# Kernel optimization log

Measured on AMD Instinct MI355X. Metric: run time of the kernel, lower is better.

Reference implementation:

```python
import jax, jax.numpy as jnp
import numpy as np
import math
from jax import lax

B, T, D, K, H, MLP_DIM, WIN = 4, 2048, 1024, 64, 4, 4096, 128
KH = K // H          # eigenstates per head
HD = D // H          # attention head dim


def layer_norm(x, g, b, eps=1e-5):
    mu = jnp.mean(x, axis=-1, keepdims=True)
    var = jnp.mean(jnp.square(x - mu), axis=-1, keepdims=True)
    return (x - mu) * lax.rsqrt(var + eps) * g + b


def setup_inputs() -> dict:
    key = jax.random.key(0)
    ks = jax.random.split(key, 16)
    s = 0.02
    # layer_idx=1, n_layers=6 -> depth_ratio=0.2, decay_center=-1.7
    return {
        "x": jax.random.normal(ks[0], (B, T, D), jnp.float32),
        "prev_eigenstates": jax.random.normal(ks[1], (B, T, 2 * K), jnp.float32),
        "norm1_g": jnp.ones((D,), jnp.float32),
        "norm1_b": jnp.zeros((D,), jnp.float32),
        "in_proj_w": jax.random.normal(ks[2], (2 * K, D), jnp.float32) * s,
        "memory_gate": jnp.array(-3.0, jnp.float32),
        "memory_proj_w": jnp.eye(2 * K, dtype=jnp.float32),
        "log_decay": jax.random.uniform(ks[3], (K,), jnp.float32, -2.7, -1.2),
        "frequency": jnp.linspace(0.0, 2 * math.pi * (1 - 1 / K), K, dtype=jnp.float32),
        "coupling": jnp.tile(jnp.eye(KH, dtype=jnp.float32), (H, 1, 1))
                    + 0.01 * jax.random.normal(ks[4], (H, KH, KH), jnp.float32) / math.sqrt(KH),
        "main_gate_w": jax.random.normal(ks[5], (D, D), jnp.float32) * s,
        "main_gate_b": jnp.full((D,), -2.0, jnp.float32),
        "out_proj_w": jax.random.normal(ks[6], (D, 2 * K), jnp.float32) * s,
        "attn_norm_g": jnp.ones((D,), jnp.float32),
        "attn_norm_b": jnp.zeros((D,), jnp.float32),
        "attn_in_w": jax.random.normal(ks[7], (3 * D, D), jnp.float32) * s,
        "attn_in_b": jnp.zeros((3 * D,), jnp.float32),
        "attn_out_w": jax.random.normal(ks[8], (D, D), jnp.float32) * s,
        "attn_out_b": jnp.zeros((D,), jnp.float32),
        "norm2_g": jnp.ones((D,), jnp.float32),
        "norm2_b": jnp.zeros((D,), jnp.float32),
        "mlp_w1": jax.random.normal(ks[9], (MLP_DIM, D), jnp.float32) * s,
        "mlp_b1": jnp.zeros((MLP_DIM,), jnp.float32),
        "mlp_w2": jax.random.normal(ks[10], (D, MLP_DIM), jnp.float32) * s,
        "mlp_b2": jnp.zeros((D,), jnp.float32),
    }


def eigenstate_fft(log_decay, frequency, beta_r, beta_i):
    # diagonal complex SSM recurrence: c_t = lam * c_{t-1} + beta_t
    lam = jnp.exp(log_decay)
    lr = lam * jnp.cos(frequency)   # (K,)
    li = lam * jnp.sin(frequency)
    br = jnp.transpose(beta_r, (1, 0, 2))  # (T,B,K)
    bi = jnp.transpose(beta_i, (1, 0, 2))

    def step(carry, inp):
        sr, si = carry
        xr, xi = inp
        nr = lr * sr - li * si + xr
        ni = lr * si + li * sr + xi
        return (nr, ni), (nr, ni)

    init = (jnp.zeros(br.shape[1:], br.dtype), jnp.zeros(bi.shape[1:], bi.dtype))
    _, (cr, ci) = lax.scan(step, init, (br, bi))
    return jnp.transpose(cr, (1, 0, 2)), jnp.transpose(ci, (1, 0, 2))


def reference(x, prev_eigenstates, norm1_g, norm1_b, in_proj_w, memory_gate,
              memory_proj_w, log_decay, frequency, coupling, main_gate_w,
              main_gate_b, out_proj_w, attn_norm_g, attn_norm_b, attn_in_w,
              attn_in_b, attn_out_w, attn_out_b, norm2_g, norm2_b,
              mlp_w1, mlp_b1, mlp_w2, mlp_b2):
    b, t, d = x.shape
    residual = x
    x_norm = layer_norm(x, norm1_g, norm1_b)

    beta = jnp.einsum('btd,kd->btk', x_norm, in_proj_w)        # (B,T,2K)
    beta_r, beta_i = jnp.split(beta, 2, axis=-1)

    # cross-layer memory
    mg = jax.nn.sigmoid(memory_gate)
    prev = jnp.einsum('btk,jk->btj', prev_eigenstates, memory_proj_w)
    pr, pi = jnp.split(prev, 2, axis=-1)
    beta_r = beta_r + mg * pr
    beta_i = beta_i + mg * pi

    c_r, c_i = eigenstate_fft(log_decay, frequency, beta_r, beta_i)  # (B,T,K)

    # per-head coupling
    c_r_h = c_r.reshape(b, t, H, KH)
    c_i_h = c_i.reshape(b, t, H, KH)
    c_r = jnp.einsum('hjk,bthk->bthj', coupling, c_r_h).reshape(b, t, K)
    c_i = jnp.einsum('hjk,bthk->bthj', coupling, c_i_h).reshape(b, t, K)
    eigenstates_out = jnp.concatenate([c_r, c_i], axis=-1)     # (B,T,2K)

    h = jnp.einsum('btk,dk->btd', eigenstates_out, out_proj_w)
    # spectral gate (band gates computed in torch are unused in the output)
    main_g = jax.nn.sigmoid(jnp.einsum('btd,ed->bte', x_norm, main_gate_w) + main_gate_b)
    h = main_g * h
    x = residual + h

    # sliding-window attention (dense masked MHA, as in the source)
    attn_in = layer_norm(x, attn_norm_g, attn_norm_b)
    qkv = jnp.einsum('btd,ed->bte', attn_in, attn_in_w) + attn_in_b
    q, k_, v = jnp.split(qkv, 3, axis=-1)
    q = q.reshape(b, t, H, HD).transpose(0, 2, 1, 3)           # (B,H,T,hd)
    k_ = k_.reshape(b, t, H, HD).transpose(0, 2, 1, 3)
    v = v.reshape(b, t, H, HD).transpose(0, 2, 1, 3)
    scale = 1.0 / math.sqrt(HD)
    scores = jnp.einsum('bhqd,bhkd->bhqk', q, k_) * scale
    idx = jnp.arange(t)
    diff = idx[:, None] - idx[None, :]
    allowed = (diff >= 0) & (diff <= WIN)                      # True = attend
    scores = jnp.where(allowed, scores, jnp.finfo(scores.dtype).min)
    attn = jax.nn.softmax(scores, axis=-1)
    ao = jnp.einsum('bhqk,bhkd->bhqd', attn, v)
    ao = ao.transpose(0, 2, 1, 3).reshape(b, t, d)
    ao = jnp.einsum('btd,ed->bte', ao, attn_out_w) + attn_out_b
    x = x + ao

    # MLP
    x2 = layer_norm(x, norm2_g, norm2_b)
    m = jax.nn.silu(jnp.einsum('btd,md->btm', x2, mlp_w1) + mlp_b1)
    m = jnp.einsum('btm,dm->btd', m, mlp_w2) + mlp_b2
    x = x + m
    return (x, eigenstates_out)
```

## Files before the change

### kernel.cpp

```cpp
#include <hip/hip_runtime.h>


typedef __bf16 bf16_t;
typedef bf16_t bf16x8 __attribute__((ext_vector_type(8)));
typedef bf16_t bf16x4 __attribute__((ext_vector_type(4)));
typedef float  f32x4  __attribute__((ext_vector_type(4)));

#define Tc   2048
#define Dc   1024
#define BTc  8192
#define K2c  128
#define MLPc 4096

struct ConvSeg { const float* src; bf16_t* dst; int n; };
struct ConvArgs { ConvSeg s[9]; };

__global__ __launch_bounds__(256) void convert_kernel(ConvArgs a) {
    ConvSeg sg = a.s[blockIdx.y];
    int i = (blockIdx.x * 256 + threadIdx.x) * 4;
    if (i >= sg.n) return;
    float4 v = *(const float4*)(sg.src + i);
    bf16x4 o;
    o[0] = (bf16_t)v.x; o[1] = (bf16_t)v.y; o[2] = (bf16_t)v.z; o[3] = (bf16_t)v.w;
    *(bf16x4*)(sg.dst + i) = o;
}

__global__ __launch_bounds__(256) void ln_kernel(const float* __restrict__ x,
                                                 const float* __restrict__ g,
                                                 const float* __restrict__ bb,
                                                 bf16_t* __restrict__ out) {
    int row = blockIdx.x;
    int tid = threadIdx.x;
    float4 v = ((const float4*)(x + (size_t)row * Dc))[tid];
    float s  = v.x + v.y + v.z + v.w;
    float ss = v.x * v.x + v.y * v.y + v.z * v.z + v.w * v.w;
#pragma unroll
    for (int d = 32; d > 0; d >>= 1) {
        s  += __shfl_down(s, d);
        ss += __shfl_down(ss, d);
    }
    __shared__ float red[8];
    int wv = tid >> 6;
    if ((tid & 63) == 0) { red[wv] = s; red[4 + wv] = ss; }
    __syncthreads();
    s  = red[0] + red[1] + red[2] + red[3];
    ss = red[4] + red[5] + red[6] + red[7];
    float mean = s * (1.0f / Dc);
    float var  = ss * (1.0f / Dc) - mean * mean;
    float rstd = rsqrtf(var + 1e-5f);
    float4 g4 = ((const float4*)g)[tid];
    float4 b4 = ((const float4*)bb)[tid];
    bf16x4 o;
    o[0] = (bf16_t)((v.x - mean) * rstd * g4.x + b4.x);
    o[1] = (bf16_t)((v.y - mean) * rstd * g4.y + b4.y);
    o[2] = (bf16_t)((v.z - mean) * rstd * g4.z + b4.z);
    o[3] = (bf16_t)((v.w - mean) * rstd * g4.w + b4.w);
    *(bf16x4*)(out + (size_t)row * Dc + tid * 4) = o;
}

#define BM 128
#define BN 128
#define BK 32

struct EpiParams {
    const float* bias;
    float*       fout;
    const float* fin;
    bf16_t*      bout;
    bf16_t*      q; bf16_t* k; bf16_t* v;
    const bf16_t* a2; const bf16_t* w2;
};

#define GLOAD_LDS(g, l)                                                        \
    __builtin_amdgcn_global_load_lds(                                          \
        (const __attribute__((address_space(1))) unsigned int*)(g),            \
        (__attribute__((address_space(3))) unsigned int*)(l), 16, 0, 0)

template <int EPI>
__global__ __launch_bounds__(256) void gemm_tiled(const bf16_t* __restrict__ A,
                                                  const bf16_t* __restrict__ W,
                                                  int M, int N, int K,
                                                  EpiParams ep) {
    __shared__ bf16_t As[BM * BK];
    __shared__ bf16_t Bs[BN * BK];

    int tid = threadIdx.x;
    int wv = tid >> 6, lane = tid & 63;
    int lane16 = lane & 15, quad = lane >> 4;
    int nbn = N / BN;
    int bm = blockIdx.x / nbn, bn = blockIdx.x % nbn;
    int m0 = bm * BM, n0 = bn * BN;
    int wm = (wv >> 1) * 64, wn = (wv & 1) * 64;

    int lrow = lane >> 2;
    int lcol = (((lane & 3) ^ ((lrow >> 1) & 3))) * 8;
    const bf16_t* ga = A + (size_t)(m0 + wv * 16 + lrow) * K + lcol;
    const bf16_t* gb = W + (size_t)(n0 + wv * 16 + lrow) * K + lcol;
    size_t gstep64 = (size_t)64 * K;
    bf16_t* la0 = &As[(wv * 16) * BK];
    bf16_t* la1 = &As[(64 + wv * 16) * BK];
    bf16_t* lb0 = &Bs[(wv * 16) * BK];
    bf16_t* lb1 = &Bs[(64 + wv * 16) * BK];

    int pc = (quad ^ ((lane16 >> 1) & 3)) * 8;

    f32x4 zz = {0.f, 0.f, 0.f, 0.f};
    f32x4 acc[4][4];
#pragma unroll
    for (int mi = 0; mi < 4; mi++)
#pragma unroll
        for (int ni = 0; ni < 4; ni++) acc[mi][ni] = zz;

    for (int k0 = 0; k0 < K; k0 += BK) {
        GLOAD_LDS(ga + k0, la0);
        GLOAD_LDS(ga + k0 + gstep64, la1);
        GLOAD_LDS(gb + k0, lb0);
        GLOAD_LDS(gb + k0 + gstep64, lb1);
        __syncthreads();
        bf16x8 af[4], bfr[4];
#pragma unroll
        for (int mi = 0; mi < 4; mi++)
            af[mi] = *(const bf16x8*)&As[(wm + mi * 16 + lane16) * BK + pc];
#pragma unroll
        for (int ni = 0; ni < 4; ni++)
            bfr[ni] = *(const bf16x8*)&Bs[(wn + ni * 16 + lane16) * BK + pc];
#pragma unroll
        for (int mi = 0; mi < 4; mi++)
#pragma unroll
            for (int ni = 0; ni < 4; ni++)
                acc[mi][ni] = __builtin_amdgcn_mfma_f32_16x16x32_bf16(
                    af[mi], bfr[ni], acc[mi][ni], 0, 0, 0);
        __syncthreads();
    }

    f32x4 acc2[4][4];
    if constexpr (EPI == 6) {
#pragma unroll
        for (int mi = 0; mi < 4; mi++)
#pragma unroll
            for (int ni = 0; ni < 4; ni++) acc2[mi][ni] = zz;
        const bf16_t* ga2 = ep.a2 + (size_t)(m0 + wv * 16 + lrow) * K2c + lcol;
        const bf16_t* gb2 = ep.w2 + (size_t)(n0 + wv * 16 + lrow) * K2c + lcol;
        size_t gstep64b = (size_t)64 * K2c;
        for (int k0 = 0; k0 < K2c; k0 += BK) {
            GLOAD_LDS(ga2 + k0, la0);
            GLOAD_LDS(ga2 + k0 + gstep64b, la1);
            GLOAD_LDS(gb2 + k0, lb0);
            GLOAD_LDS(gb2 + k0 + gstep64b, lb1);
            __syncthreads();
            bf16x8 af[4], bfr[4];
#pragma unroll
            for (int mi = 0; mi < 4; mi++)
                af[mi] = *(const bf16x8*)&As[(wm + mi * 16 + lane16) * BK + pc];
#pragma unroll
            for (int ni = 0; ni < 4; ni++)
                bfr[ni] = *(const bf16x8*)&Bs[(wn + ni * 16 + lane16) * BK + pc];
#pragma unroll
            for (int mi = 0; mi < 4; mi++)
#pragma unroll
                for (int ni = 0; ni < 4; ni++)
                    acc2[mi][ni] = __builtin_amdgcn_mfma_f32_16x16x32_bf16(
                        af[mi], bfr[ni], acc2[mi][ni], 0, 0, 0);
            __syncthreads();
        }
    }

#pragma unroll
    for (int mi = 0; mi < 4; mi++)
#pragma unroll
        for (int ni = 0; ni < 4; ni++)
#pragma unroll
            for (int r = 0; r < 4; r++) {
                int row = m0 + wm + mi * 16 + quad * 4 + r;
                int col = n0 + wn + ni * 16 + lane16;
                float v = acc[mi][ni][r];
                if constexpr (EPI == 1) {
                    v += ep.bias[col];
                    ep.bout[(size_t)row * N + col] = (bf16_t)(v / (1.0f + __expf(-v)));
                } else if constexpr (EPI == 2) {
                    size_t o = (size_t)row * N + col;
                    ep.fout[o] = ep.fin[o] + v + ep.bias[col];
                } else if constexpr (EPI == 3) {
                    v += ep.bias[col];
                    int part = col >> 10, d1 = col & 1023;
                    int hh = d1 >> 8, hd = d1 & 255;
                    int b = row >> 11, t = row & 2047;
                    bf16_t* dst = (part == 0) ? ep.q : ep.k;
                    dst[(((size_t)(b * 4 + hh) * Tc + t) << 8) + hd] = (bf16_t)v;
                } else if constexpr (EPI == 5) {
                    v += ep.bias[2048 + row];
                    int b = col >> 11, t = col & 2047;
                    int hh = row >> 8, dd = row & 255;
                    ep.v[((size_t)((b * 4 + hh) * 256 + dd)) * Tc + t] = (bf16_t)v;
                } else if constexpr (EPI == 6) {
                    size_t o = (size_t)row * N + col;
                    float g = 1.0f / (1.0f + __expf(-(v + ep.bias[col])));
                    ep.fout[o] = ep.fin[o] + g * acc2[mi][ni][r];
                }
            }
}

__device__ __forceinline__ void mm32(const bf16_t* __restrict__ A,
                                     const bf16_t* __restrict__ W,
                                     int K, int m0, int n0,
                                     int lane16, int quad, f32x4 (&acc)[2][2]) {
    const bf16_t* a0 = A + (size_t)(m0 + lane16) * K + quad * 8;
    const bf16_t* a1 = a0 + (size_t)16 * K;
    const bf16_t* w0 = W + (size_t)(n0 + lane16) * K + quad * 8;
    const bf16_t* w1 = w0 + (size_t)16 * K;
#pragma unroll 4
    for (int k = 0; k < K; k += 32) {
        bf16x8 av0 = *(const bf16x8*)(a0 + k);
        bf16x8 av1 = *(const bf16x8*)(a1 + k);
        bf16x8 bv0 = *(const bf16x8*)(w0 + k);
        bf16x8 bv1 = *(const bf16x8*)(w1 + k);
        acc[0][0] = __builtin_amdgcn_mfma_f32_16x16x32_bf16(av0, bv0, acc[0][0], 0, 0, 0);
        acc[0][1] = __builtin_amdgcn_mfma_f32_16x16x32_bf16(av0, bv1, acc[0][1], 0, 0, 0);
        acc[1][0] = __builtin_amdgcn_mfma_f32_16x16x32_bf16(av1, bv0, acc[1][0], 0, 0, 0);
        acc[1][1] = __builtin_amdgcn_mfma_f32_16x16x32_bf16(av1, bv1, acc[1][1], 0, 0, 0);
    }
}

__global__ __launch_bounds__(256) void gemm_beta(const bf16_t* __restrict__ xn,
                                                 const bf16_t* __restrict__ ipw,
                                                 const bf16_t* __restrict__ prevb,
                                                 const bf16_t* __restrict__ mpw,
                                                 const float* __restrict__ mgate_p,
                                                 float* __restrict__ beta_c) {
    int lane = threadIdx.x & 63;
    int wave = threadIdx.x >> 6;
    int gid  = blockIdx.x * 4 + wave;
    int mt = gid / 4, nt = gid % 4;
    int m0 = mt * 32, n0 = nt * 32;
    int lane16 = lane & 15, quad = lane >> 4;
    f32x4 zz = {0.f, 0.f, 0.f, 0.f};
    f32x4 acc[2][2] = {{zz, zz}, {zz, zz}};
    mm32(xn, ipw, Dc, m0, n0, lane16, quad, acc);
    f32x4 acc2[2][2] = {{zz, zz}, {zz, zz}};
    mm32(prevb, mpw, K2c, m0, n0, lane16, quad, acc2);
    float mg = 1.0f / (1.0f + __expf(-mgate_p[0]));
    for (int mi = 0; mi < 2; mi++)
        for (int ni = 0; ni < 2; ni++)
            for (int r = 0; r < 4; r++) {
                int row = m0 + mi * 16 + quad * 4 + r;
                int col = n0 + ni * 16 + lane16;
                int b = row >> 11, t = row & 2047;
                beta_c[((size_t)b * K2c + col) * Tc + t] =
                    acc[mi][ni][r] + mg * acc2[mi][ni][r];
            }
}

__global__ __launch_bounds__(64) void scan_kernel(const float* __restrict__ beta_c,
                                                  const float* __restrict__ log_decay,
                                                  const float* __restrict__ freq,
                                                  float* __restrict__ cbuf) {
    int b = blockIdx.x >> 6;
    int k = blockIdx.x & 63;
    int lane = threadIdx.x;
    float lam = expf(log_decay[k]);
    float fr = freq[k];
    float lr = lam * cosf(fr), li = lam * sinf(fr);

    const float* br_p = beta_c + ((size_t)b * K2c + k) * Tc + lane * 32;
    const float* bi_p = beta_c + ((size_t)b * K2c + 64 + k) * Tc + lane * 32;
    float br[32], bi[32];
#pragma unroll
    for (int i = 0; i < 8; i++) {
        *(float4*)(&br[i * 4]) = ((const float4*)br_p)[i];
        *(float4*)(&bi[i * 4]) = ((const float4*)bi_p)[i];
    }
    float sr = 0.f, si = 0.f;
#pragma unroll
    for (int i = 0; i < 32; i++) {
        float nr = lr * sr - li * si + br[i];
        float ni = lr * si + li * sr + bi[i];
        sr = nr; si = ni;
    }
    float Mr = lr, Mi = li;
#pragma unroll
    for (int i = 0; i < 5; i++) {
        float nr = Mr * Mr - Mi * Mi, ni = 2.f * Mr * Mi;
        Mr = nr; Mi = ni;
    }
    float ir = sr, ii = si;
#pragma unroll
    for (int d = 1; d < 64; d <<= 1) {
        float pr = __shfl_up(ir, d);
        float pi = __shfl_up(ii, d);
        if (lane >= d) {
            ir += Mr * pr - Mi * pi;
            ii += Mr * pi + Mi * pr;
        }
        float nr = Mr * Mr - Mi * Mi, ni = 2.f * Mr * Mi;
        Mr = nr; Mi = ni;
    }
    float cr = __shfl_up(ir, 1), ci = __shfl_up(ii, 1);
    if (lane == 0) { cr = 0.f; ci = 0.f; }
    float* cr_p = cbuf + ((size_t)b * K2c + k) * Tc + lane * 32;
    float* ci_p = cbuf + ((size_t)b * K2c + 64 + k) * Tc + lane * 32;
    sr = cr; si = ci;
#pragma unroll
    for (int i = 0; i < 32; i++) {
        float nr = lr * sr - li * si + br[i];
        float ni = lr * si + li * sr + bi[i];
        sr = nr; si = ni;
        cr_p[i] = sr; ci_p[i] = si;
    }
}

__global__ __launch_bounds__(256) void coupling_kernel(const float* __restrict__ cbuf,
                                                       const float* __restrict__ cpl,
                                                       float* __restrict__ eig_out,
                                                       bf16_t* __restrict__ eigb) {
    int idx = blockIdx.x * 256 + threadIdx.x;
    int col = idx & 127;
    int t = (idx >> 7) & 2047;
    int b = idx >> 18;
    int ri = col >> 6, hj = col & 63, h2 = hj >> 4, j = hj & 15;
    const float* crow = cbuf + ((size_t)b * K2c + ri * 64 + h2 * 16) * Tc + t;
    const float* cw = cpl + (h2 * 16 + j) * 16;
    float acc = 0.f;
#pragma unroll
    for (int kk = 0; kk < 16; kk++) acc += cw[kk] * crow[(size_t)kk * Tc];
    eig_out[idx] = acc;
    eigb[idx] = (bf16_t)acc;
}

#define LDP 168

__global__ __launch_bounds__(256) void attn_mfma(const bf16_t* __restrict__ qb,
                                                 const bf16_t* __restrict__ kb,
                                                 const bf16_t* __restrict__ vt,
                                                 bf16_t* __restrict__ ao) {
    __shared__ bf16_t Pl[4 * 16 * LDP];
    int tid = threadIdx.x;
    int wv = tid >> 6, lane = tid & 63;
    int lane16 = lane & 15, quad = lane >> 4;
    int qblk = blockIdx.x & 31;
    int bh = blockIdx.x >> 5;
    int qw0 = qblk * 64 + wv * 16;
    const bf16_t* qp = qb + (size_t)bh * Tc * 256;
    const bf16_t* kp = kb + (size_t)bh * Tc * 256;
    const bf16_t* vp = vt + (size_t)bh * 256 * Tc;
    bf16_t* Pw = &Pl[wv * 16 * LDP];

    for (int i = lane; i < 16 * 24; i += 64) {
        int r = i / 24, c = 144 + (i % 24);
        Pw[r * LDP + c] = (bf16_t)0.f;
    }

    bf16x8 qf[8];
#pragma unroll
    for (int ks = 0; ks < 8; ks++)
        qf[ks] = *(const bf16x8*)(qp + (size_t)(qw0 + lane16) * 256 + ks * 32 + quad * 8);

    f32x4 zz = {0.f, 0.f, 0.f, 0.f};
    f32x4 S[9];
#pragma unroll
    for (int jt = 0; jt < 9; jt++) S[jt] = zz;
    int kbase = qw0 - 128;

#pragma unroll
    for (int ks = 0; ks < 8; ks++) {
        bf16x8 kf[9];
#pragma unroll
        for (int jt = 0; jt < 9; jt++) {
            int krow = kbase + jt * 16 + lane16;
            krow = krow < 0 ? 0 : krow;
            kf[jt] = *(const bf16x8*)(kp + (size_t)krow * 256 + ks * 32 + quad * 8);
        }
#pragma unroll
        for (int jt = 0; jt < 9; jt++)
            S[jt] = __builtin_amdgcn_mfma_f32_16x16x32_bf16(qf[ks], kf[jt], S[jt], 0, 0, 0);
    }

    float m[4], l[4];
#pragma unroll
    for (int r = 0; r < 4; r++) m[r] = -1e30f;
#pragma unroll
    for (int jt = 0; jt < 9; jt++) {
        int kg = kbase + jt * 16 + lane16;
#pragma unroll
        for (int r = 0; r < 4; r++) {
            int qrow = qw0 + quad * 4 + r;
            bool ok = (kg >= 0) && (kg <= qrow) && (kg >= qrow - 128);
            float v = ok ? S[jt][r] * 0.0625f : -1e30f;
            S[jt][r] = v;
            m[r] = fmaxf(m[r], v);
        }
    }
#pragma unroll
    for (int d = 1; d < 16; d <<= 1)
#pragma unroll
        for (int r = 0; r < 4; r++)
            m[r] = fmaxf(m[r], __shfl_xor(m[r], d));
#pragma unroll
    for (int r = 0; r < 4; r++) l[r] = 0.f;
#pragma unroll
    for (int jt = 0; jt < 9; jt++)
#pragma unroll
        for (int r = 0; r < 4; r++) {
            float p = __expf(S[jt][r] - m[r]);
            S[jt][r] = p;
            l[r] += p;
        }
#pragma unroll
    for (int d = 1; d < 16; d <<= 1)
#pragma unroll
        for (int r = 0; r < 4; r++)
            l[r] += __shfl_xor(l[r], d);

#pragma unroll
    for (int jt = 0; jt < 9; jt++)
#pragma unroll
        for (int r = 0; r < 4; r++)
            Pw[(quad * 4 + r) * LDP + jt * 16 + lane16] = (bf16_t)S[jt][r];
    __syncthreads();

    f32x4 O[16];
#pragma unroll
    for (int nt = 0; nt < 16; nt++) O[nt] = zz;
#pragma unroll
    for (int ks = 0; ks < 5; ks++) {
        bf16x8 pf = *(const bf16x8*)&Pw[lane16 * LDP + ks * 32 + quad * 8];
        int kidx = kbase + ks * 32 + quad * 8;
        kidx = kidx < 0 ? 0 : kidx;
        kidx = kidx > (Tc - 8) ? (Tc - 8) : kidx;
#pragma unroll
        for (int nt = 0; nt < 16; nt++) {
            bf16x8 vf = *(const bf16x8*)(vp + (size_t)(nt * 16 + lane16) * Tc + kidx);
            O[nt] = __builtin_amdgcn_mfma_f32_16x16x32_bf16(pf, vf, O[nt], 0, 0, 0);
        }
    }

    float rl[4];
#pragma unroll
    for (int r = 0; r < 4; r++) rl[r] = 1.0f / l[r];
    int b = bh >> 2, h = bh & 3;
#pragma unroll
    for (int nt = 0; nt < 16; nt++)
#pragma unroll
        for (int r = 0; r < 4; r++) {
            int qrow = qw0 + quad * 4 + r;
            int dim = nt * 16 + lane16;
            ao[((size_t)(b * Tc + qrow)) * Dc + h * 256 + dim] = (bf16_t)(O[nt][r] * rl[r]);
        }
}

extern "C" void kernel_launch(void* const* d_in, const int* in_sizes, int n_in,
                              void* d_out, int out_size, void* d_ws, size_t ws_size,
                              hipStream_t stream) {
    const float* x            = (const float*)d_in[0];
    const float* prev_eig     = (const float*)d_in[1];
    const float* norm1_g      = (const float*)d_in[2];
    const float* norm1_b      = (const float*)d_in[3];
    const float* in_proj_w    = (const float*)d_in[4];
    const float* memory_gate  = (const float*)d_in[5];
    const float* memory_proj_w= (const float*)d_in[6];
    const float* log_decay    = (const float*)d_in[7];
    const float* frequency    = (const float*)d_in[8];
    const float* coupling     = (const float*)d_in[9];
    const float* main_gate_w  = (const float*)d_in[10];
    const float* main_gate_b  = (const float*)d_in[11];
    const float* out_proj_w   = (const float*)d_in[12];
    const float* attn_norm_g  = (const float*)d_in[13];
    const float* attn_norm_b  = (const float*)d_in[14];
    const float* attn_in_w    = (const float*)d_in[15];
    const float* attn_in_b    = (const float*)d_in[16];
    const float* attn_out_w   = (const float*)d_in[17];
    const float* attn_out_b   = (const float*)d_in[18];
    const float* norm2_g      = (const float*)d_in[19];
    const float* norm2_b      = (const float*)d_in[20];
    const float* mlp_w1       = (const float*)d_in[21];
    const float* mlp_b1       = (const float*)d_in[22];
    const float* mlp_w2       = (const float*)d_in[23];
    const float* mlp_b2       = (const float*)d_in[24];

    char* ws = (char*)d_ws;
    bf16_t* ipw_b  = (bf16_t*)(ws + 0);
    bf16_t* mpw_b  = (bf16_t*)(ws + 262144);
    bf16_t* mgw_b  = (bf16_t*)(ws + 294912);
    bf16_t* opw_b  = (bf16_t*)(ws + 2392064);
    bf16_t* aiw_b  = (bf16_t*)(ws + 2654208);
    bf16_t* aow_b  = (bf16_t*)(ws + 8945664);
    bf16_t* w1_b   = (bf16_t*)(ws + 11042816);
    bf16_t* w2_b   = (bf16_t*)(ws + 19431424);
    bf16_t* prev_b = (bf16_t*)(ws + 27820032);
    const size_t OFF_ACTA = 29917184;
    const size_t OFF_BIG  = OFF_ACTA + 16777216;
    bf16_t* actA   = (bf16_t*)(ws + OFF_ACTA);
    float*  beta_c = (float*)(ws + OFF_BIG);
    float*  cbuf   = (float*)(ws + OFF_BIG + 4194304);
    bf16_t* eigb   = (bf16_t*)(ws + OFF_BIG + 8388608);
    bf16_t* qbuf   = (bf16_t*)(ws + OFF_BIG);
    bf16_t* kbuf   = (bf16_t*)(ws + OFF_BIG + 16777216);
    bf16_t* vtbuf  = (bf16_t*)(ws + OFF_BIG + 33554432);
    bf16_t* mbuf   = (bf16_t*)(ws + OFF_BIG);

    float* out_x   = (float*)d_out;
    float* out_eig = out_x + (size_t)BTc * Dc;
    float* xres    = out_x;

    ConvArgs ca;
    ca.s[0] = ConvSeg{in_proj_w,     ipw_b,  131072};
    ca.s[1] = ConvSeg{memory_proj_w, mpw_b,  16384};
    ca.s[2] = ConvSeg{main_gate_w,   mgw_b,  1048576};
    ca.s[3] = ConvSeg{out_proj_w,    opw_b,  131072};
    ca.s[4] = ConvSeg{attn_in_w,     aiw_b,  3145728};
    ca.s[5] = ConvSeg{attn_out_w,    aow_b,  1048576};
    ca.s[6] = ConvSeg{mlp_w1,        w1_b,   4194304};
    ca.s[7] = ConvSeg{mlp_w2,        w2_b,   4194304};
    ca.s[8] = ConvSeg{prev_eig,      prev_b, 1048576};
    convert_kernel<<<dim3(4096, 9), 256, 0, stream>>>(ca);

    EpiParams ep{};

    ln_kernel<<<BTc, 256, 0, stream>>>(x, norm1_g, norm1_b, actA);
    gemm_beta<<<256, 256, 0, stream>>>(actA, ipw_b, prev_b, mpw_b, memory_gate, beta_c);
    scan_kernel<<<256, 64, 0, stream>>>(beta_c, log_decay, frequency, cbuf);
    coupling_kernel<<<4096, 256, 0, stream>>>(cbuf, coupling, out_eig, eigb);
    ep = EpiParams{}; ep.bias = main_gate_b; ep.fin = x; ep.fout = xres;
    ep.a2 = eigb; ep.w2 = opw_b;
    gemm_tiled<6><<<(BTc/BM)*(Dc/BN), 256, 0, stream>>>(actA, mgw_b, BTc, Dc, Dc, ep);
    ln_kernel<<<BTc, 256, 0, stream>>>(xres, attn_norm_g, attn_norm_b, actA);
    ep = EpiParams{}; ep.bias = attn_in_b; ep.q = qbuf; ep.k = kbuf;
    gemm_tiled<3><<<(BTc/BM)*(2048/BN), 256, 0, stream>>>(actA, aiw_b, BTc, 2048, Dc, ep);
    ep = EpiParams{}; ep.bias = attn_in_b; ep.v = vtbuf;
    gemm_tiled<5><<<(Dc/BM)*(BTc/BN), 256, 0, stream>>>(aiw_b + (size_t)2048 * Dc, actA,
                                                        Dc, BTc, Dc, ep);
    attn_mfma<<<512, 256, 0, stream>>>(qbuf, kbuf, vtbuf, actA);
    ep = EpiParams{}; ep.bias = attn_out_b; ep.fin = xres; ep.fout = xres;
    gemm_tiled<2><<<(BTc/BM)*(Dc/BN), 256, 0, stream>>>(actA, aow_b, BTc, Dc, Dc, ep);
    ln_kernel<<<BTc, 256, 0, stream>>>(xres, norm2_g, norm2_b, actA);
    ep = EpiParams{}; ep.bias = mlp_b1; ep.bout = mbuf;
    gemm_tiled<1><<<(BTc/BM)*(MLPc/BN), 256, 0, stream>>>(actA, w1_b, BTc, MLPc, Dc, ep);
    ep = EpiParams{}; ep.bias = mlp_b2; ep.fin = xres; ep.fout = out_x;
    gemm_tiled<2><<<(BTc/BM)*(Dc/BN), 256, 0, stream>>>(mbuf, w2_b, BTc, Dc, MLPc, ep);

    (void)in_sizes; (void)n_in; (void)out_size; (void)ws_size;
}
```

Measured before the change: 699.2 us.

## Double GEMM K-tile to 64 with 8-way XOR swizzle and XCD-aware block mapping

```diff
diff --git a/kernel.cpp b/kernel.cpp
--- a/kernel.cpp
+++ b/kernel.cpp
@@ -60,7 +60,7 @@
 
 #define BM 128
 #define BN 128
-#define BK 32
+#define BKT 64
 
 struct EpiParams {
     const float* bias;
@@ -81,28 +81,29 @@
                                                   const bf16_t* __restrict__ W,
                                                   int M, int N, int K,
                                                   EpiParams ep) {
-    __shared__ bf16_t As[BM * BK];
-    __shared__ bf16_t Bs[BN * BK];
+    __shared__ bf16_t As[BM * BKT];
+    __shared__ bf16_t Bs[BN * BKT];
 
     int tid = threadIdx.x;
     int wv = tid >> 6, lane = tid & 63;
     int lane16 = lane & 15, quad = lane >> 4;
-    int nbn = N / BN;
-    int bm = blockIdx.x / nbn, bn = blockIdx.x % nbn;
+    int nbn = N / BN, nbm = M / BM;
+
+    int bid = blockIdx.x;
+    int xcd = bid & 7;
+    int slot = bid >> 3;
+    int bm_per = nbm >> 3;
+    int bmo = slot / nbn;
+    int bno = slot % nbn;
+    if (bmo & 1) bno = nbn - 1 - bno;
+    int bm = xcd * bm_per + bmo, bn = bno;
     int m0 = bm * BM, n0 = bn * BN;
     int wm = (wv >> 1) * 64, wn = (wv & 1) * 64;
 
-    int lrow = lane >> 2;
-    int lcol = (((lane & 3) ^ ((lrow >> 1) & 3))) * 8;
-    const bf16_t* ga = A + (size_t)(m0 + wv * 16 + lrow) * K + lcol;
-    const bf16_t* gb = W + (size_t)(n0 + wv * 16 + lrow) * K + lcol;
-    size_t gstep64 = (size_t)64 * K;
-    bf16_t* la0 = &As[(wv * 16) * BK];
-    bf16_t* la1 = &As[(64 + wv * 16) * BK];
-    bf16_t* lb0 = &Bs[(wv * 16) * BK];
-    bf16_t* lb1 = &Bs[(64 + wv * 16) * BK];
-
-    int pc = (quad ^ ((lane16 >> 1) & 3)) * 8;
+    int lrow = lane >> 3;
+    int lcol = ((lane & 7) ^ lrow) * 8;
+    const bf16_t* ga = A + (size_t)(m0 + wv * 32 + lrow) * K + lcol;
+    const bf16_t* gb = W + (size_t)(n0 + wv * 32 + lrow) * K + lcol;
 
     f32x4 zz = {0.f, 0.f, 0.f, 0.f};
     f32x4 acc[4][4];
@@ -111,25 +112,31 @@
 #pragma unroll
         for (int ni = 0; ni < 4; ni++) acc[mi][ni] = zz;
 
-    for (int k0 = 0; k0 < K; k0 += BK) {
-        GLOAD_LDS(ga + k0, la0);
-        GLOAD_LDS(ga + k0 + gstep64, la1);
-        GLOAD_LDS(gb + k0, lb0);
-        GLOAD_LDS(gb + k0 + gstep64, lb1);
+    for (int k0 = 0; k0 < K; k0 += BKT) {
+#pragma unroll
+        for (int j = 0; j < 4; j++) {
+            GLOAD_LDS(ga + k0 + (size_t)(j * 8) * K, &As[(wv * 32 + j * 8) * BKT]);
+            GLOAD_LDS(gb + k0 + (size_t)(j * 8) * K, &Bs[(wv * 32 + j * 8) * BKT]);
+        }
         __syncthreads();
-        bf16x8 af[4], bfr[4];
-#pragma unroll
-        for (int mi = 0; mi < 4; mi++)
-            af[mi] = *(const bf16x8*)&As[(wm + mi * 16 + lane16) * BK + pc];
-#pragma unroll
-        for (int ni = 0; ni < 4; ni++)
-            bfr[ni] = *(const bf16x8*)&Bs[(wn + ni * 16 + lane16) * BK + pc];
-#pragma unroll
-        for (int mi = 0; mi < 4; mi++)
+#pragma unroll
+        for (int ks = 0; ks < 2; ks++) {
+            bf16x8 af[4], bfr[4];
+#pragma unroll
+            for (int mi = 0; mi < 4; mi++)
+                af[mi] = *(const bf16x8*)&As[(wm + mi * 16 + lane16) * BKT +
+                                             (((ks * 4 + quad) ^ (lane16 & 7)) * 8)];
 #pragma unroll
             for (int ni = 0; ni < 4; ni++)
-                acc[mi][ni] = __builtin_amdgcn_mfma_f32_16x16x32_bf16(
-                    af[mi], bfr[ni], acc[mi][ni], 0, 0, 0);
+                bfr[ni] = *(const bf16x8*)&Bs[(wn + ni * 16 + lane16) * BKT +
+                                              (((ks * 4 + quad) ^ (lane16 & 7)) * 8)];
+#pragma unroll
+            for (int mi = 0; mi < 4; mi++)
+#pragma unroll
+                for (int ni = 0; ni < 4; ni++)
+                    acc[mi][ni] = __builtin_amdgcn_mfma_f32_16x16x32_bf16(
+                        af[mi], bfr[ni], acc[mi][ni], 0, 0, 0);
+        }
         __syncthreads();
     }
 
@@ -139,28 +146,33 @@
         for (int mi = 0; mi < 4; mi++)
 #pragma unroll
             for (int ni = 0; ni < 4; ni++) acc2[mi][ni] = zz;
-        const bf16_t* ga2 = ep.a2 + (size_t)(m0 + wv * 16 + lrow) * K2c + lcol;
-        const bf16_t* gb2 = ep.w2 + (size_t)(n0 + wv * 16 + lrow) * K2c + lcol;
-        size_t gstep64b = (size_t)64 * K2c;
-        for (int k0 = 0; k0 < K2c; k0 += BK) {
-            GLOAD_LDS(ga2 + k0, la0);
-            GLOAD_LDS(ga2 + k0 + gstep64b, la1);
-            GLOAD_LDS(gb2 + k0, lb0);
-            GLOAD_LDS(gb2 + k0 + gstep64b, lb1);
+        const bf16_t* ga2 = ep.a2 + (size_t)(m0 + wv * 32 + lrow) * K2c + lcol;
+        const bf16_t* gb2 = ep.w2 + (size_t)(n0 + wv * 32 + lrow) * K2c + lcol;
+        for (int k0 = 0; k0 < K2c; k0 += BKT) {
+#pragma unroll
+            for (int j = 0; j < 4; j++) {
+                GLOAD_LDS(ga2 + k0 + (size_t)(j * 8) * K2c, &As[(wv * 32 + j * 8) * BKT]);
+                GLOAD_LDS(gb2 + k0 + (size_t)(j * 8) * K2c, &Bs[(wv * 32 + j * 8) * BKT]);
+            }
             __syncthreads();
-            bf16x8 af[4], bfr[4];
-#pragma unroll
-            for (int mi = 0; mi < 4; mi++)
-                af[mi] = *(const bf16x8*)&As[(wm + mi * 16 + lane16) * BK + pc];
-#pragma unroll
-            for (int ni = 0; ni < 4; ni++)
-                bfr[ni] = *(const bf16x8*)&Bs[(wn + ni * 16 + lane16) * BK + pc];
-#pragma unroll
-            for (int mi = 0; mi < 4; mi++)
+#pragma unroll
+            for (int ks = 0; ks < 2; ks++) {
+                bf16x8 af[4], bfr[4];
+#pragma unroll
+                for (int mi = 0; mi < 4; mi++)
+                    af[mi] = *(const bf16x8*)&As[(wm + mi * 16 + lane16) * BKT +
+                                                 (((ks * 4 + quad) ^ (lane16 & 7)) * 8)];
 #pragma unroll
                 for (int ni = 0; ni < 4; ni++)
-                    acc2[mi][ni] = __builtin_amdgcn_mfma_f32_16x16x32_bf16(
-                        af[mi], bfr[ni], acc2[mi][ni], 0, 0, 0);
+                    bfr[ni] = *(const bf16x8*)&Bs[(wn + ni * 16 + lane16) * BKT +
+                                                  (((ks * 4 + quad) ^ (lane16 & 7)) * 8)];
+#pragma unroll
+                for (int mi = 0; mi < 4; mi++)
+#pragma unroll
+                    for (int ni = 0; ni < 4; ni++)
+                        acc2[mi][ni] = __builtin_amdgcn_mfma_f32_16x16x32_bf16(
+                            af[mi], bfr[ni], acc2[mi][ni], 0, 0, 0);
+            }
             __syncthreads();
         }
     }
```

Measured after the change: 640.7 us. -8.4%, faster.
